# Kernel optimization log

Measured on AMD Instinct MI355X. Metric: run time of the kernel, lower is better.

## Reference

```python
import jax, jax.numpy as jnp
import numpy as np

N = 100000   # nodes
E = 1600000  # edges (before self loops)
G = 256      # graphs in batch
F = 128      # feature_size
H = 128      # hidden_channels
L = 3        # num_layers - 1 GAT layers
NC1 = 10     # task1 classes
GF = 8       # graph_feature_size
EPS = 1e-5


def _bn_pack(key, C):
    kg, kb, km, kv = jax.random.split(key, 4)
    gamma = jax.random.uniform(kg, (C,), minval=0.5, maxval=1.5)
    beta = jax.random.normal(kb, (C,)) * 0.1
    mean = jax.random.normal(km, (C,)) * 0.1
    var = jax.random.uniform(kv, (C,), minval=0.5, maxval=1.5)
    return jnp.stack([gamma, beta, mean, var]).astype(jnp.float32)  # [4, C]


def setup_inputs() -> dict:
    key = jax.random.key(0)
    ks = jax.random.split(key, 24)
    x = jax.random.normal(ks[0], (N, F), dtype=jnp.float32)
    edge_index = jax.random.randint(ks[1], (2, E), 0, N)
    batch_ids = jnp.sort(jax.random.randint(ks[2], (N,), 0, G))
    graph_features = jax.random.normal(ks[3], (G, GF), dtype=jnp.float32)
    s = 0.05
    gat_W = jax.random.normal(ks[4], (L, F, H), dtype=jnp.float32) * s
    gat_att_src = jax.random.normal(ks[5], (L, H), dtype=jnp.float32) * s
    gat_att_dst = jax.random.normal(ks[6], (L, H), dtype=jnp.float32) * s
    gat_bias = jax.random.normal(ks[7], (L, H), dtype=jnp.float32) * 0.01
    bn_emb = _bn_pack(ks[8], H)
    bn_t1 = _bn_pack(ks[9], NC1)
    bn_comb = _bn_pack(ks[10], H + 5)
    fc1_w = jax.random.normal(ks[11], (H + 1, NC1), dtype=jnp.float32) * s
    fc1_b = jax.random.normal(ks[12], (NC1,), dtype=jnp.float32) * s
    fc2_w = jax.random.normal(ks[13], (H + 3, 2), dtype=jnp.float32) * s
    fc2_b = jax.random.normal(ks[14], (2,), dtype=jnp.float32) * s
    fc3a_w = jax.random.normal(ks[15], (H + 5, 4), dtype=jnp.float32) * s
    fc3a_b = jax.random.normal(ks[16], (4,), dtype=jnp.float32) * s
    fc3b_w = jax.random.normal(ks[17], (H + 5, 5), dtype=jnp.float32) * s
    fc3b_b = jax.random.normal(ks[18], (5,), dtype=jnp.float32) * s
    return dict(x=x, edge_index=edge_index, batch_ids=batch_ids,
                graph_features=graph_features, task=0,
                gat_W=gat_W, gat_att_src=gat_att_src, gat_att_dst=gat_att_dst,
                gat_bias=gat_bias, bn_emb=bn_emb, bn_t1=bn_t1, bn_comb=bn_comb,
                fc1_w=fc1_w, fc1_b=fc1_b, fc2_w=fc2_w, fc2_b=fc2_b,
                fc3a_w=fc3a_w, fc3a_b=fc3a_b, fc3b_w=fc3b_w, fc3b_b=fc3b_b)


def _bn_eval(x, pack):
    gamma, beta, mean, var = pack
    return (x - mean) * gamma * jax.lax.rsqrt(var + EPS) + beta


def _gat_layer(x, W, a_src, a_dst, b, src, dst):
    h = x @ W                              # [N, H]
    e_src = (h @ a_src)[src]               # [Etot]
    e_dst = (h @ a_dst)[dst]
    e = jax.nn.leaky_relu(e_src + e_dst, negative_slope=0.2)
    emax = jax.ops.segment_max(e, dst, num_segments=N)
    ee = jnp.exp(e - emax[dst])
    denom = jax.ops.segment_sum(ee, dst, num_segments=N)
    alpha = ee / denom[dst]                # edge softmax per destination node
    out = jax.ops.segment_sum(h[src] * alpha[:, None], dst, num_segments=N)
    return out + b


def _forward(x, edge_index, batch_ids, graph_features,
             gat_W, gat_att_src, gat_att_dst, gat_bias,
             bn_emb, bn_t1, bn_comb,
             fc1_w, fc1_b, fc2_w, fc2_b, fc3a_w, fc3a_b, fc3b_w, fc3b_b):
    loops = jnp.arange(N)
    src = jnp.concatenate([edge_index[0], loops])  # PyG GATConv adds self-loops
    dst = jnp.concatenate([edge_index[1], loops])
    for i in range(L):
        x = jax.nn.relu(_gat_layer(x, gat_W[i], gat_att_src[i], gat_att_dst[i],
                                   gat_bias[i], src, dst))
    # global mean pool over graphs
    sums = jax.ops.segment_sum(x, batch_ids, num_segments=G)
    cnt = jax.ops.segment_sum(jnp.ones((N,), x.dtype), batch_ids, num_segments=G)
    x = sums / jnp.maximum(cnt, 1.0)[:, None]
    x = _bn_eval(x, bn_emb)
    lev_lsb = graph_features[:, -1:]
    nx_feats = graph_features[:, -3:]
    out1 = jnp.concatenate([x, lev_lsb], axis=1) @ fc1_w + fc1_b
    out1 = _bn_eval(jax.nn.relu(out1), bn_t1)
    out2 = jax.nn.relu(jnp.concatenate([x, nx_feats], axis=1) @ fc2_w + fc2_b)
    pred2 = jnp.argmax(out2, axis=1)
    wf1 = graph_features[:, 2:3]
    wf2 = graph_features[:, 1:2]
    x3 = _bn_eval(jnp.concatenate([x, wf1, wf2, nx_feats], axis=1), bn_comb)
    b1 = x3 @ fc3a_w + fc3a_b              # [G, 4]
    b2 = x3 @ fc3b_w + fc3b_b              # [G, 5]
    m0 = (pred2 == 0)[:, None].astype(x.dtype)
    m1 = (pred2 == 1)[:, None].astype(x.dtype)
    out3 = jnp.concatenate([b1 * m0, b2 * m1], axis=1)  # [G, 9]
    return out1, out2, out3


def reference(x, edge_index, batch_ids, graph_features, task,
              gat_W, gat_att_src, gat_att_dst, gat_bias,
              bn_emb, bn_t1, bn_comb,
              fc1_w, fc1_b, fc2_w, fc2_b, fc3a_w, fc3a_b, fc3b_w, fc3b_b):
    return _forward(x, edge_index, batch_ids, graph_features,
                    gat_W, gat_att_src, gat_att_dst, gat_bias,
                    bn_emb, bn_t1, bn_comb,
                    fc1_w, fc1_b, fc2_w, fc2_b, fc3a_w, fc3a_b, fc3b_w, fc3b_b)
```

## Files before the change

### kernel.cpp

```cpp
#include <hip/hip_runtime.h>
#include <math.h>

#define Nn 100000
#define Ee 1600000
#define Mm (Ee + Nn)
#define Gg 256
#define EPSf 1e-5f
#define NB 391
#define EPB 4096
#define NEB 391
#define PCAP 8192

typedef _Float16 f16x8 __attribute__((ext_vector_type(8)));
typedef _Float16 half4_t __attribute__((ext_vector_type(4)));
typedef float f32x4 __attribute__((ext_vector_type(4)));


__global__ void k_prepW(const float* __restrict__ W, _Float16* __restrict__ Wt,
                        int* __restrict__ gtail) {
  int l = blockIdx.x;
  if (l < 3) {
    const float* w = W + (size_t)l * 16384;
    _Float16* wt = Wt + (size_t)l * 16384;
    for (int i = threadIdx.x; i < 16384; i += 256) {
      int k = i >> 7, c = i & 127;
      wt[c * 128 + k] = (_Float16)w[i];
    }
  } else {
    for (int i = threadIdx.x; i < NB; i += 256) gtail[i] = 0;
  }
}


__global__ __launch_bounds__(256) void k_bin(const int* __restrict__ src,
                                             const int* __restrict__ dst,
                                             int* __restrict__ gtail,
                                             int* __restrict__ pairs, int e) {
  __shared__ int lcnt[NB];
  __shared__ int lbase[NB];
  int t = threadIdx.x;
  for (int i = t; i < NB; i += 256) lcnt[i] = 0;
  __syncthreads();
  int base = blockIdx.x * EPB;
  int pk[EPB / 256], br[EPB / 256], bk[EPB / 256];
  #pragma unroll
  for (int i = 0; i < EPB / 256; ++i) {
    int idx = base + i * 256 + t;
    if (idx < e) {
      int d = dst[idx];
      pk[i] = (src[idx] << 8) | (d & 255);
      bk[i] = d >> 8;
      br[i] = atomicAdd(&lcnt[bk[i]], 1);
    } else br[i] = -1;
  }
  __syncthreads();
  for (int i = t; i < NB; i += 256)
    if (lcnt[i] > 0) lbase[i] = atomicAdd(&gtail[i], lcnt[i]);
  __syncthreads();
  #pragma unroll
  for (int i = 0; i < EPB / 256; ++i) {
    if (br[i] >= 0) {
      int pos = lbase[bk[i]] + br[i];
      if (pos < PCAP) pairs[bk[i] * PCAP + pos] = pk[i];
    }
  }
}

__global__ __launch_bounds__(512) void k_bscan(const int* __restrict__ gtail,
                                               int* __restrict__ bbase,
                                               int* __restrict__ rp) {
  __shared__ int s2[512];
  int t = threadIdx.x;
  int c = (t < NB) ? min(gtail[t], PCAP) : 0;
  int nib = (t < NB) ? min(Nn - (t << 8), 256) : 0;
  int tot = c + nib;
  s2[t] = tot;
  __syncthreads();
  for (int o = 1; o < 512; o <<= 1) {
    int u = (t >= o) ? s2[t - o] : 0;
    __syncthreads(); s2[t] += u; __syncthreads();
  }
  if (t < NB) bbase[t] = s2[t] - tot;
  if (t == 511) rp[Nn] = s2[511];
}

__global__ __launch_bounds__(256) void k_place(const int* __restrict__ pairs,
                                               const int* __restrict__ gtail,
                                               const int* __restrict__ bbase,
                                               int* __restrict__ rp,
                                               int* __restrict__ csr) {
  __shared__ int cnt[256];
  __shared__ int ofs[256];
  int b = blockIdx.x, t = threadIdx.x;
  int v0 = b << 8;
  int nib = min(Nn - v0, 256);
  int pb = b * PCAP;
  int pc = min(gtail[b], PCAP);
  int cb = bbase[b];
  cnt[t] = (t < nib) ? 1 : 0;
  __syncthreads();
  for (int j = t; j < pc; j += 256) {
    atomicAdd(&cnt[pairs[pb + j] & 255], 1);
  }
  __syncthreads();
  int c = cnt[t];
  ofs[t] = c;
  __syncthreads();
  for (int o = 1; o < 256; o <<= 1) {
    int u = (t >= o) ? ofs[t - o] : 0;
    __syncthreads(); ofs[t] += u; __syncthreads();
  }
  int excl = ofs[t] - c;
  if (t < nib) rp[v0 + t] = cb + excl;
  cnt[t] = excl;
  __syncthreads();
  if (t < nib) {
    int pos = atomicAdd(&cnt[t], 1);
    csr[cb + pos] = v0 + t;
  }
  __syncthreads();
  for (int j = t; j < pc; j += 256) {
    int p = pairs[pb + j];
    int pos = atomicAdd(&cnt[p & 255], 1);
    csr[cb + pos] = p >> 8;
  }
}


template<bool F32IN>
__global__ __launch_bounds__(256) void k_gemm(const void* __restrict__ Xv,
                                              const _Float16* __restrict__ Wt,
                                              const float* __restrict__ asrc,
                                              const float* __restrict__ adst,
                                              _Float16* __restrict__ H,
                                              float* __restrict__ es,
                                              float* __restrict__ ed, int n) {
  int wid = threadIdx.x >> 6;
  int lane = threadIdx.x & 63;
  int r0 = blockIdx.x * 128 + wid * 32;
  if (r0 >= n) return;
  int lo16 = lane & 15, q = lane >> 4;

  f32x4 acc0[8] = {};
  f32x4 acc1[8] = {};
  const _Float16* wb = Wt + (size_t)lo16 * 128 + q * 8;

  #pragma unroll
  for (int kk = 0; kk < 4; ++kk) {
    f16x8 b0, b1;
    if constexpr (F32IN) {
      const float* xf = (const float*)Xv + (size_t)(r0 + lo16) * 128 + q * 8 + kk * 32;
      float4 u0 = *reinterpret_cast<const float4*>(xf);
      float4 u1 = *reinterpret_cast<const float4*>(xf + 4);
      float4 v0 = *reinterpret_cast<const float4*>(xf + 16 * 128);
      float4 v1 = *reinterpret_cast<const float4*>(xf + 16 * 128 + 4);
      b0 = f16x8{(_Float16)u0.x, (_Float16)u0.y, (_Float16)u0.z, (_Float16)u0.w,
                 (_Float16)u1.x, (_Float16)u1.y, (_Float16)u1.z, (_Float16)u1.w};
      b1 = f16x8{(_Float16)v0.x, (_Float16)v0.y, (_Float16)v0.z, (_Float16)v0.w,
                 (_Float16)v1.x, (_Float16)v1.y, (_Float16)v1.z, (_Float16)v1.w};
    } else {
      const _Float16* xh = (const _Float16*)Xv + (size_t)(r0 + lo16) * 128 + q * 8 + kk * 32;
      b0 = *reinterpret_cast<const f16x8*>(xh);
      b1 = *reinterpret_cast<const f16x8*>(xh + 16 * 128);
    }
    #pragma unroll
    for (int c = 0; c < 8; ++c) {
      f16x8 a = *reinterpret_cast<const f16x8*>(wb + (size_t)c * 2048 + kk * 32);
      acc0[c] = __builtin_amdgcn_mfma_f32_16x16x32_f16(a, b0, acc0[c], 0, 0, 0);
      acc1[c] = __builtin_amdgcn_mfma_f32_16x16x32_f16(a, b1, acc1[c], 0, 0, 0);
    }
  }

  float es0 = 0.f, es1 = 0.f, ed0 = 0.f, ed1 = 0.f;
  #pragma unroll
  for (int c = 0; c < 8; ++c) {
    float4 as = reinterpret_cast<const float4*>(asrc)[c * 4 + q];
    float4 ad = reinterpret_cast<const float4*>(adst)[c * 4 + q];
    es0 += acc0[c][0] * as.x + acc0[c][1] * as.y + acc0[c][2] * as.z + acc0[c][3] * as.w;
    ed0 += acc0[c][0] * ad.x + acc0[c][1] * ad.y + acc0[c][2] * ad.z + acc0[c][3] * ad.w;
    es1 += acc1[c][0] * as.x + acc1[c][1] * as.y + acc1[c][2] * as.z + acc1[c][3] * as.w;
    ed1 += acc1[c][0] * ad.x + acc1[c][1] * ad.y + acc1[c][2] * ad.z + acc1[c][3] * ad.w;
  }
  es0 += __shfl_xor(es0, 16); es0 += __shfl_xor(es0, 32);
  ed0 += __shfl_xor(ed0, 16); ed0 += __shfl_xor(ed0, 32);
  es1 += __shfl_xor(es1, 16); es1 += __shfl_xor(es1, 32);
  ed1 += __shfl_xor(ed1, 16); ed1 += __shfl_xor(ed1, 32);

  half4_t* H4 = reinterpret_cast<half4_t*>(H);
  int row0 = r0 + lo16;
  #pragma unroll
  for (int c = 0; c < 8; ++c) {
    half4_t h0 = { (_Float16)acc0[c][0], (_Float16)acc0[c][1],
                   (_Float16)acc0[c][2], (_Float16)acc0[c][3] };
    half4_t h1 = { (_Float16)acc1[c][0], (_Float16)acc1[c][1],
                   (_Float16)acc1[c][2], (_Float16)acc1[c][3] };
    H4[(size_t)row0 * 32 + c * 4 + q]        = h0;
    H4[(size_t)(row0 + 16) * 32 + c * 4 + q] = h1;
  }
  if (lane < 16) {
    es[r0 + lane] = es0;       ed[r0 + lane] = ed0;
    es[r0 + 16 + lane] = es1;  ed[r0 + 16 + lane] = ed1;
  }
}


__global__ __launch_bounds__(256) void k_agg(const _Float16* __restrict__ H,
                                             const int* __restrict__ rp,
                                             const int* __restrict__ csr,
                                             const float* __restrict__ es,
                                             const float* __restrict__ ed,
                                             const float* __restrict__ bias,
                                             _Float16* __restrict__ Xo, int n) {
  int v = blockIdx.x * 4 + (threadIdx.x >> 6);
  if (v >= n) return;
  int lane = threadIdx.x & 63;
  int g = lane >> 4;
  int s = lane & 15;
  int r0 = rp[v], r1 = rp[v + 1];
  int deg = r1 - r0;
  float edv = ed[v];
  const f16x8* H8 = reinterpret_cast<const f16x8*>(H);
  float acc[8] = {};
  float inv;

  if (deg <= 64) {
    int u = 0;
    float e = -3.0e38f;
    if (lane < deg) {
      u = csr[r0 + lane];
      e = es[u] + edv;
      e = e > 0.f ? e : 0.2f * e;
    }
    float m = e;
    #pragma unroll
    for (int o = 32; o; o >>= 1) m = fmaxf(m, __shfl_xor(m, o));
    float pw = (lane < deg) ? __expf(e - m) : 0.f;
    float den = pw;
    #pragma unroll
    for (int o = 32; o; o >>= 1) den += __shfl_xor(den, o);
    inv = 1.f / den;

    int niter = (deg + 3) >> 2;
    int uu = __shfl(u, g);
    float ww = __shfl(pw, g);
    f16x8 hv = H8[uu * 16 + s];
    #pragma unroll 2
    for (int i = 1; i < niter; ++i) {
      int idx = 4 * i + g;
      int uu2 = __shfl(u, idx);
      float ww2 = __shfl(pw, idx);
      f16x8 hv2 = H8[uu2 * 16 + s];
      #pragma unroll
      for (int k2 = 0; k2 < 8; ++k2) acc[k2] += ww * (float)hv[k2];
      ww = ww2; hv = hv2;
    }
    #pragma unroll
    for (int k2 = 0; k2 < 8; ++k2) acc[k2] += ww * (float)hv[k2];
  } else {
    float m = -3.0e38f;
    for (int j = r0 + lane; j < r1; j += 64) {
      float e = es[csr[j]] + edv;
      e = e > 0.f ? e : 0.2f * e;
      m = fmaxf(m, e);
    }
    #pragma unroll
    for (int o = 32; o; o >>= 1) m = fmaxf(m, __shfl_xor(m, o));
    float den = 0.f;
    for (int j = r0 + lane; j < r1; j += 64) {
      float e = es[csr[j]] + edv;
      e = e > 0.f ? e : 0.2f * e;
      den += __expf(e - m);
    }
    #pragma unroll
    for (int o = 32; o; o >>= 1) den += __shfl_xor(den, o);
    inv = 1.f / den;
    for (int j = r0; j < r1; j += 4) {
      int idx = j + g;
      if (idx < r1) {
        int uu = csr[idx];
        float e = es[uu] + edv;
        e = e > 0.f ? e : 0.2f * e;
        float ww = __expf(e - m);
        f16x8 hv = H8[uu * 16 + s];
        #pragma unroll
        for (int k2 = 0; k2 < 8; ++k2) acc[k2] += ww * (float)hv[k2];
      }
    }
  }
  #pragma unroll
  for (int k2 = 0; k2 < 8; ++k2) {
    acc[k2] += __shfl_xor(acc[k2], 16);
    acc[k2] += __shfl_xor(acc[k2], 32);
  }
  if (lane < 16) {
    float4 b0 = reinterpret_cast<const float4*>(bias)[s * 2];
    float4 b1 = reinterpret_cast<const float4*>(bias)[s * 2 + 1];
    f16x8 o;
    o[0] = (_Float16)fmaxf(acc[0] * inv + b0.x, 0.f);
    o[1] = (_Float16)fmaxf(acc[1] * inv + b0.y, 0.f);
    o[2] = (_Float16)fmaxf(acc[2] * inv + b0.z, 0.f);
    o[3] = (_Float16)fmaxf(acc[3] * inv + b0.w, 0.f);
    o[4] = (_Float16)fmaxf(acc[4] * inv + b1.x, 0.f);
    o[5] = (_Float16)fmaxf(acc[5] * inv + b1.y, 0.f);
    o[6] = (_Float16)fmaxf(acc[6] * inv + b1.z, 0.f);
    o[7] = (_Float16)fmaxf(acc[7] * inv + b1.w, 0.f);
    reinterpret_cast<f16x8*>(Xo)[v * 16 + s] = o;
  }
}


__global__ __launch_bounds__(512) void k_poolheads(
    const _Float16* __restrict__ X16, const int* __restrict__ batch,
    const float* __restrict__ bn_emb, const float* __restrict__ gf,
    const float* __restrict__ bn_t1, const float* __restrict__ bn_comb,
    const float* __restrict__ fc1w, const float* __restrict__ fc1b,
    const float* __restrict__ fc2w, const float* __restrict__ fc2b,
    const float* __restrict__ fc3aw, const float* __restrict__ fc3ab,
    const float* __restrict__ fc3bw, const float* __restrict__ fc3bb,
    float* __restrict__ out, int n) {
  __shared__ float4 part[16][32];
  __shared__ float xs[128];
  __shared__ float x3[133];
  __shared__ float o2[2];
  int g = blockIdx.x, t = threadIdx.x;
  int s = t & 31;
  int way = t >> 5;
  int lo = 0, hi = n;
  while (lo < hi) { int mid = (lo + hi) >> 1; if (batch[mid] < g) lo = mid + 1; else hi = mid; }
  int s0 = lo;
  lo = s0; hi = n;
  while (lo < hi) { int mid = (lo + hi) >> 1; if (batch[mid] < g + 1) lo = mid + 1; else hi = mid; }
  int e0 = lo;
  const half4_t* X4 = reinterpret_cast<const half4_t*>(X16);
  float4 acc = make_float4(0.f, 0.f, 0.f, 0.f);
  for (int i = s0 + way; i < e0; i += 16) {
    half4_t h = X4[(size_t)i * 32 + s];
    acc.x += (float)h[0]; acc.y += (float)h[1];
    acc.z += (float)h[2]; acc.w += (float)h[3];
  }
  part[way][s] = acc;
  __syncthreads();
  if (way == 0) {
    float4 tt = part[0][s];
    #pragma unroll
    for (int w = 1; w < 16; ++w) {
      float4 u = part[w][s];
      tt.x += u.x; tt.y += u.y; tt.z += u.z; tt.w += u.w;
    }
    float invc = (e0 > s0) ? 1.f / (float)(e0 - s0) : 0.f;
    int c0 = s * 4;
    #pragma unroll
    for (int k = 0; k < 4; ++k) {
      float mean = ((const float*)&tt)[k] * invc;
      int c = c0 + k;
      float gm = bn_emb[c], bt = bn_emb[128 + c], mu = bn_emb[256 + c], vr = bn_emb[384 + c];
      xs[c] = (mean - mu) * gm * rsqrtf(vr + EPSf) + bt;
    }
  }
  __syncthreads();

  const float* gfg = &gf[g * 8];
  float lev = gfg[7];
  float nx0 = gfg[5], nx1 = gfg[6], nx2 = gfg[7];
  float wf1 = gfg[2], wf2 = gfg[1];
  if (t < 10) {
    float o = fc1b[t];
    for (int k = 0; k < 128; ++k) o += xs[k] * fc1w[k * 10 + t];
    o += lev * fc1w[128 * 10 + t];
    o = fmaxf(o, 0.f);
    float gm = bn_t1[t], bt = bn_t1[10 + t], mu = bn_t1[20 + t], vr = bn_t1[30 + t];
    out[g * 10 + t] = (o - mu) * gm * rsqrtf(vr + EPSf) + bt;
  }
  if (t >= 10 && t < 12) {
    int j = t - 10;
    float o = fc2b[j];
    for (int k = 0; k < 128; ++k) o += xs[k] * fc2w[k * 2 + j];
    o += nx0 * fc2w[128 * 2 + j] + nx1 * fc2w[129 * 2 + j] + nx2 * fc2w[130 * 2 + j];
    o = fmaxf(o, 0.f);
    o2[j] = o;
    out[2560 + g * 2 + j] = o;
  }
  if (t >= 12 && t < 145) {
    int k = t - 12;
    float vsrc = (k < 128) ? xs[k]
               : (k == 128) ? wf1
               : (k == 129) ? wf2
               : (k == 130) ? nx0
               : (k == 131) ? nx1 : nx2;
    float gm = bn_comb[k], bt = bn_comb[133 + k], mu = bn_comb[266 + k], vr = bn_comb[399 + k];
    x3[k] = (vsrc - mu) * gm * rsqrtf(vr + EPSf) + bt;
  }
  __syncthreads();
  bool pred1 = o2[1] > o2[0];
  if (t < 4) {
    float o = fc3ab[t];
    for (int k = 0; k < 133; ++k) o += x3[k] * fc3aw[k * 4 + t];
    out[3072 + g * 9 + t] = pred1 ? 0.f : o;
  }
  if (t >= 4 && t < 9) {
    int j = t - 4;
    float o = fc3bb[j];
    for (int k = 0; k < 133; ++k) o += x3[k] * fc3bw[k * 5 + j];
    out[3072 + g * 9 + 4 + j] = pred1 ? o : 0.f;
  }
}


extern "C" void kernel_launch(void* const* d_in, const int* in_sizes, int n_in,
                              void* d_out, int out_size, void* d_ws, size_t ws_size,
                              hipStream_t stream) {
  const float* x      = (const float*)d_in[0];
  const int*   ei     = (const int*)d_in[1];
  const int*   batch  = (const int*)d_in[2];
  const float* gf     = (const float*)d_in[3];
  const float* gatW   = (const float*)d_in[5];
  const float* asrc   = (const float*)d_in[6];
  const float* adst   = (const float*)d_in[7];
  const float* gbias  = (const float*)d_in[8];
  const float* bn_emb = (const float*)d_in[9];
  const float* bn_t1  = (const float*)d_in[10];
  const float* bn_cb  = (const float*)d_in[11];
  const float* fc1w = (const float*)d_in[12]; const float* fc1b = (const float*)d_in[13];
  const float* fc2w = (const float*)d_in[14]; const float* fc2b = (const float*)d_in[15];
  const float* fc3aw = (const float*)d_in[16]; const float* fc3ab = (const float*)d_in[17];
  const float* fc3bw = (const float*)d_in[18]; const float* fc3bb = (const float*)d_in[19];
  float* out = (float*)d_out;

  char* p = (char*)d_ws;
  auto alloc = [&](size_t bytes) -> void* {
    void* r = (void*)p;
    p += (bytes + 255) & ~(size_t)255;
    return r;
  };
  _Float16* xfA  = (_Float16*)alloc((size_t)Nn * 128 * 2);
  _Float16* xfB  = (_Float16*)alloc((size_t)Nn * 128 * 2);
  _Float16* hbuf = (_Float16*)alloc((size_t)Nn * 128 * 2);
  _Float16* wt   = (_Float16*)alloc((size_t)3 * 16384 * 2);
  int*   pairs = (int*)alloc((size_t)NB * PCAP * 4);
  int*   csr  = (int*)alloc((size_t)Mm * 4);
  int*   rp   = (int*)alloc((size_t)(Nn + 1) * 4);
  int*   gtail = (int*)alloc((size_t)NB * 4);
  int*   bbase = (int*)alloc((size_t)NB * 4);
  float* es   = (float*)alloc((size_t)Nn * 4);
  float* ed   = (float*)alloc((size_t)Nn * 4);
  if ((size_t)(p - (char*)d_ws) > ws_size) return;

  const int* srcp = ei;
  const int* dstp = ei + Ee;

  k_prepW<<<4, 256, 0, stream>>>(gatW, wt, gtail);

  k_bin<<<NEB, 256, 0, stream>>>(srcp, dstp, gtail, pairs, Ee);
  k_bscan<<<1, 512, 0, stream>>>(gtail, bbase, rp);
  k_place<<<NB, 256, 0, stream>>>(pairs, gtail, bbase, rp, csr);

  int ngrid = (Nn + 127) / 128;
  k_gemm<true><<<ngrid, 256, 0, stream>>>(x, wt, asrc, adst, hbuf, es, ed, Nn);
  k_agg<<<(Nn + 3) / 4, 256, 0, stream>>>(hbuf, rp, csr, es, ed, gbias, xfA, Nn);
  k_gemm<false><<<ngrid, 256, 0, stream>>>(xfA, wt + 16384, asrc + 128, adst + 128,
                                           hbuf, es, ed, Nn);
  k_agg<<<(Nn + 3) / 4, 256, 0, stream>>>(hbuf, rp, csr, es, ed, gbias + 128, xfB, Nn);
  k_gemm<false><<<ngrid, 256, 0, stream>>>(xfB, wt + 32768, asrc + 256, adst + 256,
                                           hbuf, es, ed, Nn);
  k_agg<<<(Nn + 3) / 4, 256, 0, stream>>>(hbuf, rp, csr, es, ed, gbias + 256, xfA, Nn);

  k_poolheads<<<Gg, 512, 0, stream>>>(xfA, batch, bn_emb, gf, bn_t1, bn_cb,
                                      fc1w, fc1b, fc2w, fc2b, fc3aw, fc3ab,
                                      fc3bw, fc3bb, out, Nn);
}
```

Before: 507.9 us.

## Process two nodes per wavefront in GAT aggregation and fold block scan into placement

The aggregation kernel now gives each 32-lane half of a wavefront its own destination node whenever both nodes have degree at most 32. This halves the wavefront count and cuts idle lanes for the typical average degree of about 17. Higher-degree pairs fall back to a serial per-node path that uses the full wavefront. Separately, the single-block bucket scan kernel is removed and each placement block computes its own prefix base by reducing over all bucket counts. That saves a launch but adds redundant work in every block.

```diff
diff --git a/kernel.cpp b/kernel.cpp
--- a/kernel.cpp
+++ b/kernel.cpp
@@ -66,37 +66,34 @@
   }
 }
 
-__global__ __launch_bounds__(512) void k_bscan(const int* __restrict__ gtail,
-                                               int* __restrict__ bbase,
-                                               int* __restrict__ rp) {
-  __shared__ int s2[512];
-  int t = threadIdx.x;
-  int c = (t < NB) ? min(gtail[t], PCAP) : 0;
-  int nib = (t < NB) ? min(Nn - (t << 8), 256) : 0;
-  int tot = c + nib;
-  s2[t] = tot;
-  __syncthreads();
-  for (int o = 1; o < 512; o <<= 1) {
-    int u = (t >= o) ? s2[t - o] : 0;
-    __syncthreads(); s2[t] += u; __syncthreads();
-  }
-  if (t < NB) bbase[t] = s2[t] - tot;
-  if (t == 511) rp[Nn] = s2[511];
-}
-
 __global__ __launch_bounds__(256) void k_place(const int* __restrict__ pairs,
                                                const int* __restrict__ gtail,
-                                               const int* __restrict__ bbase,
                                                int* __restrict__ rp,
                                                int* __restrict__ csr) {
+  __shared__ int red[256];
   __shared__ int cnt[256];
   __shared__ int ofs[256];
   int b = blockIdx.x, t = threadIdx.x;
+  int myb = 0, mya = 0;
+  for (int i = t; i < NB; i += 256) {
+    int ci = min(gtail[i], PCAP) + min(Nn - (i << 8), 256);
+    mya += ci;
+    if (i < b) myb += ci;
+  }
+  red[t] = myb; __syncthreads();
+  for (int o = 128; o; o >>= 1) { if (t < o) red[t] += red[t + o]; __syncthreads(); }
+  int cb = red[0];
+  __syncthreads();
+  if (b == NB - 1) {
+    red[t] = mya; __syncthreads();
+    for (int o = 128; o; o >>= 1) { if (t < o) red[t] += red[t + o]; __syncthreads(); }
+    if (t == 0) rp[Nn] = red[0];
+    __syncthreads();
+  }
   int v0 = b << 8;
   int nib = min(Nn - v0, 256);
   int pb = b * PCAP;
   int pc = min(gtail[b], PCAP);
-  int cb = bbase[b];
   cnt[t] = (t < nib) ? 1 : 0;
   __syncthreads();
   for (int j = t; j < pc; j += 256) {
@@ -211,42 +208,47 @@
                                              const float* __restrict__ ed,
                                              const float* __restrict__ bias,
                                              _Float16* __restrict__ Xo, int n) {
-  int v = blockIdx.x * 4 + (threadIdx.x >> 6);
-  if (v >= n) return;
+  int w = blockIdx.x * 4 + (threadIdx.x >> 6);
   int lane = threadIdx.x & 63;
-  int g = lane >> 4;
+  int half = lane >> 5;
+  int l32 = lane & 31;
   int s = lane & 15;
-  int r0 = rp[v], r1 = rp[v + 1];
-  int deg = r1 - r0;
-  float edv = ed[v];
   const f16x8* H8 = reinterpret_cast<const f16x8*>(H);
   float acc[8] = {};
+
+  int v = w * 2 + half;
+  int vc = (v < n) ? v : (n - 1);
+  int r0 = rp[vc], r1 = rp[vc + 1];
+  int deg = r1 - r0;
+  float edv = ed[vc];
   float inv;
-
-  if (deg <= 64) {
+  int vstore = v;
+
+  if (__all(deg <= 32)) {
     int u = 0;
     float e = -3.0e38f;
-    if (lane < deg) {
-      u = csr[r0 + lane];
+    if (l32 < deg) {
+      u = csr[r0 + l32];
       e = es[u] + edv;
       e = e > 0.f ? e : 0.2f * e;
     }
     float m = e;
     #pragma unroll
-    for (int o = 32; o; o >>= 1) m = fmaxf(m, __shfl_xor(m, o));
-    float pw = (lane < deg) ? __expf(e - m) : 0.f;
+    for (int o = 16; o; o >>= 1) m = fmaxf(m, __shfl_xor(m, o));
+    float pw = (l32 < deg) ? __expf(e - m) : 0.f;
     float den = pw;
     #pragma unroll
-    for (int o = 32; o; o >>= 1) den += __shfl_xor(den, o);
+    for (int o = 16; o; o >>= 1) den += __shfl_xor(den, o);
     inv = 1.f / den;
 
-    int niter = (deg + 3) >> 2;
-    int uu = __shfl(u, g);
-    float ww = __shfl(pw, g);
-    f16x8 hv = H8[uu * 16 + s];
+    int g2 = (lane >> 4) & 1;
+    int hb = half << 5;
+    int niter = (deg + 1) >> 1;
+    float ww = __shfl(pw, hb + g2);
+    f16x8 hv = H8[__shfl(u, hb + g2) * 16 + s];
     #pragma unroll 2
     for (int i = 1; i < niter; ++i) {
-      int idx = 4 * i + g;
+      int idx = hb + 2 * i + g2;
       int uu2 = __shfl(u, idx);
       float ww2 = __shfl(pw, idx);
       f16x8 hv2 = H8[uu2 * 16 + s];
@@ -256,43 +258,93 @@
     }
     #pragma unroll
     for (int k2 = 0; k2 < 8; ++k2) acc[k2] += ww * (float)hv[k2];
+    #pragma unroll
+    for (int k2 = 0; k2 < 8; ++k2) acc[k2] += __shfl_xor(acc[k2], 16);
   } else {
-    float m = -3.0e38f;
-    for (int j = r0 + lane; j < r1; j += 64) {
-      float e = es[csr[j]] + edv;
-      e = e > 0.f ? e : 0.2f * e;
-      m = fmaxf(m, e);
-    }
-    #pragma unroll
-    for (int o = 32; o; o >>= 1) m = fmaxf(m, __shfl_xor(m, o));
-    float den = 0.f;
-    for (int j = r0 + lane; j < r1; j += 64) {
-      float e = es[csr[j]] + edv;
-      e = e > 0.f ? e : 0.2f * e;
-      den += __expf(e - m);
-    }
-    #pragma unroll
-    for (int o = 32; o; o >>= 1) den += __shfl_xor(den, o);
-    inv = 1.f / den;
-    for (int j = r0; j < r1; j += 4) {
-      int idx = j + g;
-      if (idx < r1) {
-        int uu = csr[idx];
-        float e = es[uu] + edv;
-        e = e > 0.f ? e : 0.2f * e;
-        float ww = __expf(e - m);
-        f16x8 hv = H8[uu * 16 + s];
+    float invA = 1.f, invB = 1.f;
+    float accA[8] = {}, accB[8] = {};
+    #pragma unroll
+    for (int t2 = 0; t2 < 2; ++t2) {
+      int vv = w * 2 + t2;
+      if (vv >= n) break;
+      int rr0 = __shfl(r0, t2 * 32), rr1 = __shfl(r1, t2 * 32);
+      int dg = rr1 - rr0;
+      float edvv = __shfl(edv, t2 * 32);
+      float* ac = t2 ? accB : accA;
+      int g4 = lane >> 4;
+      float iv;
+      if (dg <= 64) {
+        int u = 0;
+        float e = -3.0e38f;
+        if (lane < dg) {
+          u = csr[rr0 + lane];
+          e = es[u] + edvv;
+          e = e > 0.f ? e : 0.2f * e;
+        }
+        float m = e;
         #pragma unroll
-        for (int k2 = 0; k2 < 8; ++k2) acc[k2] += ww * (float)hv[k2];
+        for (int o = 32; o; o >>= 1) m = fmaxf(m, __shfl_xor(m, o));
+        float pw = (lane < dg) ? __expf(e - m) : 0.f;
+        float den = pw;
+        #pragma unroll
+        for (int o = 32; o; o >>= 1) den += __shfl_xor(den, o);
+        iv = 1.f / den;
+        int niter = (dg + 3) >> 2;
+        for (int i = 0; i < niter; ++i) {
+          int idx = 4 * i + g4;
+          int uu = __shfl(u, idx);
+          float ww = __shfl(pw, idx);
+          f16x8 hv = H8[uu * 16 + s];
+          #pragma unroll
+          for (int k2 = 0; k2 < 8; ++k2) ac[k2] += ww * (float)hv[k2];
+        }
+      } else {
+        float m = -3.0e38f;
+        for (int j = rr0 + lane; j < rr1; j += 64) {
+          float e = es[csr[j]] + edvv;
+          e = e > 0.f ? e : 0.2f * e;
+          m = fmaxf(m, e);
+        }
+        #pragma unroll
+        for (int o = 32; o; o >>= 1) m = fmaxf(m, __shfl_xor(m, o));
+        float den = 0.f;
+        for (int j = rr0 + lane; j < rr1; j += 64) {
+          float e = es[csr[j]] + edvv;
+          e = e > 0.f ? e : 0.2f * e;
+          den += __expf(e - m);
+        }
+        #pragma unroll
+        for (int o = 32; o; o >>= 1) den += __shfl_xor(den, o);
+        iv = 1.f / den;
+        for (int j = rr0; j < rr1; j += 4) {
+          int idx = j + g4;
+          if (idx < rr1) {
+            int uu = csr[idx];
+            float e = es[uu] + edvv;
+            e = e > 0.f ? e : 0.2f * e;
+            float ww = __expf(e - m);
+            f16x8 hv = H8[uu * 16 + s];
+            #pragma unroll
+            for (int k2 = 0; k2 < 8; ++k2) ac[k2] += ww * (float)hv[k2];
+          }
+        }
       }
-    }
-  }
-  #pragma unroll
-  for (int k2 = 0; k2 < 8; ++k2) {
-    acc[k2] += __shfl_xor(acc[k2], 16);
-    acc[k2] += __shfl_xor(acc[k2], 32);
-  }
-  if (lane < 16) {
+      #pragma unroll
+      for (int k2 = 0; k2 < 8; ++k2) {
+        ac[k2] += __shfl_xor(ac[k2], 16);
+        ac[k2] += __shfl_xor(ac[k2], 32);
+      }
+      if (t2) invB = iv; else invA = iv;
+    }
+    #pragma unroll
+    for (int k2 = 0; k2 < 8; ++k2) {
+      float bval = __shfl(accB[k2], l32);
+      acc[k2] = half ? bval : accA[k2];
+    }
+    inv = half ? invB : invA;
+  }
+
+  if (((lane & 31) < 16) && vstore < n) {
     float4 b0 = reinterpret_cast<const float4*>(bias)[s * 2];
     float4 b1 = reinterpret_cast<const float4*>(bias)[s * 2 + 1];
     f16x8 o;
@@ -304,7 +356,7 @@
     o[5] = (_Float16)fmaxf(acc[5] * inv + b1.y, 0.f);
     o[6] = (_Float16)fmaxf(acc[6] * inv + b1.z, 0.f);
     o[7] = (_Float16)fmaxf(acc[7] * inv + b1.w, 0.f);
-    reinterpret_cast<f16x8*>(Xo)[v * 16 + s] = o;
+    reinterpret_cast<f16x8*>(Xo)[vstore * 16 + s] = o;
   }
 }
 
@@ -440,7 +492,6 @@
   int*   csr  = (int*)alloc((size_t)Mm * 4);
   int*   rp   = (int*)alloc((size_t)(Nn + 1) * 4);
   int*   gtail = (int*)alloc((size_t)NB * 4);
-  int*   bbase = (int*)alloc((size_t)NB * 4);
   float* es   = (float*)alloc((size_t)Nn * 4);
   float* ed   = (float*)alloc((size_t)Nn * 4);
   if ((size_t)(p - (char*)d_ws) > ws_size) return;
@@ -451,18 +502,18 @@
   k_prepW<<<4, 256, 0, stream>>>(gatW, wt, gtail);
 
   k_bin<<<NEB, 256, 0, stream>>>(srcp, dstp, gtail, pairs, Ee);
-  k_bscan<<<1, 512, 0, stream>>>(gtail, bbase, rp);
-  k_place<<<NB, 256, 0, stream>>>(pairs, gtail, bbase, rp, csr);
+  k_place<<<NB, 256, 0, stream>>>(pairs, gtail, rp, csr);
 
   int ngrid = (Nn + 127) / 128;
+  int agrid = (Nn + 7) / 8;
   k_gemm<true><<<ngrid, 256, 0, stream>>>(x, wt, asrc, adst, hbuf, es, ed, Nn);
-  k_agg<<<(Nn + 3) / 4, 256, 0, stream>>>(hbuf, rp, csr, es, ed, gbias, xfA, Nn);
+  k_agg<<<agrid, 256, 0, stream>>>(hbuf, rp, csr, es, ed, gbias, xfA, Nn);
   k_gemm<false><<<ngrid, 256, 0, stream>>>(xfA, wt + 16384, asrc + 128, adst + 128,
                                            hbuf, es, ed, Nn);
-  k_agg<<<(Nn + 3) / 4, 256, 0, stream>>>(hbuf, rp, csr, es, ed, gbias + 128, xfB, Nn);
+  k_agg<<<agrid, 256, 0, stream>>>(hbuf, rp, csr, es, ed, gbias + 128, xfB, Nn);
   k_gemm<false><<<ngrid, 256, 0, stream>>>(xfB, wt + 32768, asrc + 256, adst + 256,
                                            hbuf, es, ed, Nn);
-  k_agg<<<(Nn + 3) / 4, 256, 0, stream>>>(hbuf, rp, csr, es, ed, gbias + 256, xfA, Nn);
+  k_agg<<<agrid, 256, 0, stream>>>(hbuf, rp, csr, es, ed, gbias + 256, xfA, Nn);
 
   k_poolheads<<<Gg, 512, 0, stream>>>(xfA, batch, bn_emb, gf, bn_t1, bn_cb,
                                       fc1w, fc1b, fc2w, fc2b, fc3aw, fc3ab,
```

Result: no change. 501.4 us (-1.3%).
